# Optimization experiments

Hardware: AMD Instinct MI355X
Metric: run time of the kernel (lower is better)

Reference implementation:

```python
import jax, jax.numpy as jnp
import numpy as np

B, L, DIM = 2, 2048, 512
HEADS, R, W, EH, T = 8, 8, 4, 16, 2
HD = DIM // HEADS  # 64
ROPE_BASE = 10000.0


def _local_window_edges(L, w):
    pos = np.arange(L)
    offs = np.concatenate([np.arange(-w, 0), np.arange(1, w + 1)])
    tg = pos[:, None] + offs[None, :]
    valid = (tg >= 0) & (tg < L)
    ii, _ = np.nonzero(valid)          # row-major, matches torch nonzero order
    return ii.astype(np.int32), tg[valid].astype(np.int32)


def setup_inputs() -> dict:
    key = jax.random.key(0)
    ks = jax.random.split(key, 12)
    sd = 0.02
    edge_i, edge_j = _local_window_edges(L, W)
    inp = {
        "x": jax.random.normal(ks[0], (B, L, DIM), jnp.float32),
        "edge_i": jnp.asarray(edge_i),
        "edge_j": jnp.asarray(edge_j),
        "te_w": jax.random.normal(ks[1], (DIM, DIM), jnp.float32) * sd,
        "te_b": jnp.zeros((DIM,), jnp.float32),
        "a1_w": jax.random.normal(ks[2], (2 * DIM, EH), jnp.float32) * sd,
        "a1_b": jnp.zeros((EH,), jnp.float32),
        "a2_w": jax.random.normal(ks[3], (EH, 1), jnp.float32) * sd,
        "a2_b": jnp.zeros((1,), jnp.float32),
        "l1_w": jax.random.normal(ks[4], (2 * DIM, EH), jnp.float32) * sd,
        "l1_b": jnp.zeros((EH,), jnp.float32),
        "l2_w": jax.random.normal(ks[5], (EH, HEADS * R * HD), jnp.float32) * sd,
        "l2_b": jnp.zeros((HEADS * R * HD,), jnp.float32),
        "step_sizes": jnp.full((T, L), -2.2, jnp.float32),
        "out_w": jax.random.normal(ks[6], (DIM, DIM), jnp.float32) * sd,
        "out_b": jnp.zeros((DIM,), jnp.float32),
    }
    return inp


def _rope_cos_sin(rel_pos):
    # rel_pos: [E] int -> cos/sin [E, HD] (rotate-half convention)
    inv_freq = 1.0 / (ROPE_BASE ** (jnp.arange(0, HD, 2, dtype=jnp.float32) / HD))
    ang = rel_pos.astype(jnp.float32)[:, None] * inv_freq[None, :]  # [E, HD/2]
    ang = jnp.concatenate([ang, ang], axis=-1)                      # [E, HD]
    return jnp.cos(ang), jnp.sin(ang)


def _rotate_half(x):
    x1, x2 = x[..., : HD // 2], x[..., HD // 2:]
    return jnp.concatenate([-x2, x1], axis=-1)


def reference(x, edge_i, edge_j, te_w, te_b, a1_w, a1_b, a2_w, a2_b,
              l1_w, l1_b, l2_w, l2_b, step_sizes, out_w, out_b):
    E = edge_i.shape[0]
    # token encoder -> heads: u [B, H, L, HD]
    u = (x @ te_w + te_b).reshape(B, L, HEADS, HD).transpose(0, 2, 1, 3)

    # edge features from raw x: [B, E, 2*DIM]
    ef = jnp.concatenate([x[:, edge_i], x[:, edge_j]], axis=-1)
    # alpha: softplus MLP -> [B, E]
    h = jax.nn.gelu(ef @ a1_w + a1_b, approximate=False)
    alphas = jax.nn.softplus((h @ a2_w + a2_b)[..., 0])
    # Lambda: MLP -> [B, E, H, R, HD], L2-normalized on last dim
    h2 = jax.nn.gelu(ef @ l1_w + l1_b, approximate=False)
    Lam = (h2 @ l2_w + l2_b).reshape(B, E, HEADS, R, HD)
    Lam = Lam / jnp.maximum(jnp.linalg.norm(Lam, axis=-1, keepdims=True), 1e-12)

    cos, sin = _rope_cos_sin(edge_i - edge_j)  # [E, HD] each

    for t in range(T):
        eta = jax.nn.softplus(step_sizes[t])[None, None, :, None]  # [1,1,L,1]
        u_i = u[:, :, edge_i]                                      # [B,H,E,HD]
        u_j = u[:, :, edge_j]
        u_i = u_i * cos + _rotate_half(u_i) * sin
        diff = u_i - u_j
        ld = jnp.einsum('behrd,bhed->bher', Lam, diff)
        residual = alphas[:, None, :, None] * diff + jnp.einsum('bher,behrd->bhed', ld, Lam)
        upd = jnp.zeros_like(u).at[:, :, edge_i, :].add(residual)
        upd = upd.at[:, :, edge_j, :].add(-residual)
        u = u - eta * upd

    u = u.transpose(0, 2, 1, 3).reshape(B, L, DIM)
    return u @ out_w + out_b
```

## Files before the change

kernel.cpp:

```cpp
#include <hip/hip_runtime.h>
#include <hip/hip_bf16.h>

#define B_   2
#define L_   2048
#define DIM_ 512
#define NH_  8
#define HD_  64
#define R_   8
#define EH_  16
#define T_   2

__device__ __forceinline__ float gelu_f(float x){
  return 0.5f * x * (1.0f + erff(x * 0.70710678118654752f));
}
__device__ __forceinline__ float softplus_f(float x){
  return (x > 20.f) ? x : log1pf(expf(x));
}
__device__ __forceinline__ constexpr int off_of(int o){ return (o < 4) ? o - 4 : o - 3; }

__global__ __launch_bounds__(256) void k_misc(
    const float* __restrict__ l2w, const float* __restrict__ l2b,
    const float* __restrict__ step,
    float* __restrict__ W2, float* __restrict__ eta,
    float* __restrict__ ropeC, float* __restrict__ ropeS,
    int* __restrict__ esrc, int* __restrict__ edst)
{
  int idx = blockIdx.x * 256 + threadIdx.x;
  if (idx < NH_*144*64){
    int d = idx & 63;
    int n = (idx >> 6) % 144;
    int h = idx / (144*64);
    int k = n >> 3, r = n & 7;
    int col = h*512 + r*64 + d;
    float v = 0.f;
    if (k < 16) v = l2w[k*4096 + col];
    else if (k == 16) v = l2b[col];
    W2[idx] = v;
    return;
  }
  idx -= NH_*144*64;
  if (idx < T_*L_){ eta[idx] = softplus_f(step[idx]); return; }
  idx -= T_*L_;
  if (idx < 9*32){
    int d = idx & 31, rel = (idx >> 5) - 4;
    float invf = expf(-((float)d / 32.f) * 9.210340371976184f);
    float ang = (float)rel * invf;
    ropeC[idx] = cosf(ang); ropeS[idx] = sinf(ang);
    return;
  }
  idx -= 9*32;
  if (idx < 2*8*L_){
    if (idx < 8*L_) esrc[idx] = -1; else edst[idx - 8*L_] = -1;
    return;
  }
}

__global__ __launch_bounds__(256) void k_gram(
    const float* __restrict__ W2, float* __restrict__ Gram)
{
  int idx = blockIdx.x * 256 + threadIdx.x;
  if (idx >= 8*8*17*17) return;
  int bq = idx % 17;
  int a  = (idx / 17) % 17;
  int r  = (idx / 289) & 7;
  int h  = idx / (289*8);
  const float* wa = W2 + ((size_t)(h*144 + a*8 + r))*64;
  const float* wb = W2 + ((size_t)(h*144 + bq*8 + r))*64;
  float s = 0.f;
  #pragma unroll 8
  for (int d = 0; d < 64; d++) s = fmaf(wa[d], wb[d], s);
  Gram[idx] = s;
}

__global__ __launch_bounds__(256) void k_fill(
    const int* __restrict__ ei, const int* __restrict__ ej, int E,
    int* __restrict__ esrc, int* __restrict__ edst)
{
  int e = blockIdx.x * 256 + threadIdx.x;
  if (e >= E) return;
  int i = ei[e], j = ej[e];
  int o = j - i;
  int slot = (o < 0) ? (o + 4) : (o + 3);
  esrc[slot*L_ + i] = e;
  edst[slot*L_ + j] = e;
}

__global__ __launch_bounds__(256) void k_te(
    const float* __restrict__ x, const float* __restrict__ w,
    const float* __restrict__ bias, float* __restrict__ u)
{
  __shared__ float As[16][64];
  __shared__ float Bs[16][64];
  const int m0 = blockIdx.x * 64;
  const int n0 = blockIdx.y * 64;
  const int tid = threadIdx.x;
  const int ty = tid >> 4, tx = tid & 15;
  float acc[4][4] = {};
  for (int k0 = 0; k0 < 512; k0 += 16){
    {
      int m = tid >> 2, seg = tid & 3;
      float4 v = *(const float4*)(x + (size_t)(m0 + m)*512 + k0 + seg*4);
      As[seg*4+0][m] = v.x; As[seg*4+1][m] = v.y;
      As[seg*4+2][m] = v.z; As[seg*4+3][m] = v.w;
    }
    {
      int k = tid >> 4, c = (tid & 15)*4;
      float4 v = *(const float4*)(w + (size_t)(k0 + k)*512 + n0 + c);
      *(float4*)&Bs[k][c] = v;
    }
    __syncthreads();
    #pragma unroll
    for (int k = 0; k < 16; k++){
      float4 a = *(const float4*)(&As[k][ty*4]);
      float4 b = *(const float4*)(&Bs[k][tx*4]);
      float av[4] = {a.x, a.y, a.z, a.w};
      float bv[4] = {b.x, b.y, b.z, b.w};
      #pragma unroll
      for (int ii = 0; ii < 4; ii++)
        #pragma unroll
        for (int jj = 0; jj < 4; jj++)
          acc[ii][jj] = fmaf(av[ii], bv[jj], acc[ii][jj]);
    }
    __syncthreads();
  }
  const int bb = m0 >> 11;
  const int lb = (m0 & 2047) + ty*4;
  #pragma unroll
  for (int jj = 0; jj < 4; jj++){
    int n = n0 + tx*4 + jj;
    float bv = bias[n];
    float4 o;
    o.x = acc[0][jj] + bv; o.y = acc[1][jj] + bv;
    o.z = acc[2][jj] + bv; o.w = acc[3][jj] + bv;
    *(float4*)&u[((size_t)(bb*512 + n))*2048 + lb] = o;
  }
}

__global__ __launch_bounds__(256) void k_pq(
    const float* __restrict__ x, const float* __restrict__ a1w,
    const float* __restrict__ l1w, float* __restrict__ PQ)
{
  __shared__ float As[16][64];
  __shared__ float Bs[16][64];
  const int m0 = blockIdx.x * 64;
  const int tid = threadIdx.x;
  const int ty = tid >> 4, tx = tid & 15;
  const int c = (tid & 15) * 4;
  const int group = c >> 4;
  const float* src = (group & 2) ? l1w : a1w;
  const int krow_off = (group & 1) ? 512 : 0;
  const int cc = c & 15;
  float acc[4][4] = {};
  for (int k0 = 0; k0 < 512; k0 += 16){
    {
      int m = tid >> 2, seg = tid & 3;
      float4 v = *(const float4*)(x + (size_t)(m0 + m)*512 + k0 + seg*4);
      As[seg*4+0][m] = v.x; As[seg*4+1][m] = v.y;
      As[seg*4+2][m] = v.z; As[seg*4+3][m] = v.w;
    }
    {
      int k = tid >> 4;
      float4 v = *(const float4*)(src + (size_t)(krow_off + k0 + k)*16 + cc);
      *(float4*)&Bs[k][c] = v;
    }
    __syncthreads();
    #pragma unroll
    for (int k = 0; k < 16; k++){
      float4 a = *(const float4*)(&As[k][ty*4]);
      float4 b = *(const float4*)(&Bs[k][tx*4]);
      float av[4] = {a.x, a.y, a.z, a.w};
      float bv[4] = {b.x, b.y, b.z, b.w};
      #pragma unroll
      for (int ii = 0; ii < 4; ii++)
        #pragma unroll
        for (int jj = 0; jj < 4; jj++)
          acc[ii][jj] = fmaf(av[ii], bv[jj], acc[ii][jj]);
    }
    __syncthreads();
  }
  #pragma unroll
  for (int ii = 0; ii < 4; ii++){
    int m = m0 + ty*4 + ii;
    float4 o;
    o.x = acc[ii][0]; o.y = acc[ii][1]; o.z = acc[ii][2]; o.w = acc[ii][3];
    *(float4*)&PQ[(size_t)m*64 + tx*4] = o;
  }
}

__global__ __launch_bounds__(256) void k_feat2(
    const float* __restrict__ PQ, const int* __restrict__ ei, const int* __restrict__ ej,
    const float* __restrict__ a1b, const float* __restrict__ a2w,
    const float* __restrict__ a2b, const float* __restrict__ l1b,
    int E, float* __restrict__ alphas, float* __restrict__ h2e)
{
  int e = blockIdx.x * 256 + threadIdx.x;
  int b = blockIdx.y;
  if (e >= E) return;
  int i = ei[e], j = ej[e];
  const float* Pi = PQ + ((size_t)b*L_ + i)*64;
  const float* Pj = PQ + ((size_t)b*L_ + j)*64;
  float ha[16], hl[16];
  #pragma unroll
  for (int q = 0; q < 4; q++){
    float4 p1 = *(const float4*)(Pi + q*4);
    float4 q1 = *(const float4*)(Pj + 16 + q*4);
    float4 p2 = *(const float4*)(Pi + 32 + q*4);
    float4 q2 = *(const float4*)(Pj + 48 + q*4);
    ha[q*4+0] = p1.x + q1.x; ha[q*4+1] = p1.y + q1.y;
    ha[q*4+2] = p1.z + q1.z; ha[q*4+3] = p1.w + q1.w;
    hl[q*4+0] = p2.x + q2.x; hl[q*4+1] = p2.y + q2.y;
    hl[q*4+2] = p2.z + q2.z; hl[q*4+3] = p2.w + q2.w;
  }
  float av = a2b[0];
  #pragma unroll
  for (int n = 0; n < 16; n++){
    float g = gelu_f(ha[n] + a1b[n]);
    av += g * a2w[n];
  }
  alphas[(size_t)b*E + e] = softplus_f(av);
  float* he = h2e + ((size_t)b*E + e)*16;
  #pragma unroll
  for (int n = 0; n < 16; n++){
    float g = gelu_f(hl[n] + l1b[n]);
    he[n] = g;
  }
}

__global__ __launch_bounds__(256) void k_norm(
    const float* __restrict__ Gram, const float* __restrict__ h2e,
    int E, float* __restrict__ ivsq)
{
  __shared__ float Gl[8*289];
  __shared__ float Hl[256*17];
  const int tid = threadIdx.x;
  const int bh = blockIdx.y;
  const int b = bh >> 3, h = bh & 7;
  const int eb = blockIdx.x*256;
  for (int it = tid; it < 2312; it += 256) Gl[it] = Gram[(size_t)h*2312 + it];
  {
    int ge = eb + tid;
    const float* hp = h2e + ((size_t)b*E + (ge < E ? ge : 0))*16;
    #pragma unroll
    for (int q = 0; q < 4; q++){
      float4 v = *(const float4*)(hp + q*4);
      Hl[tid*17+q*4+0]=v.x; Hl[tid*17+q*4+1]=v.y;
      Hl[tid*17+q*4+2]=v.z; Hl[tid*17+q*4+3]=v.w;
    }
    Hl[tid*17+16] = 1.f;
  }
  __syncthreads();
  int ge = eb + tid;
  if (ge >= E) return;
  float m17[17];
  #pragma unroll
  for (int k = 0; k < 17; k++) m17[k] = Hl[tid*17+k];
  float* ig = ivsq + ((size_t)bh*E + ge)*8;
  #pragma unroll
  for (int r = 0; r < 8; r++){
    float ss = 0.f;
    for (int a = 0; a < 17; a++){
      float ma = Hl[tid*17 + a];
      const float* Gr = Gl + r*289 + a*17;
      float inner = 0.f;
      #pragma unroll
      for (int bq = 0; bq < 17; bq++)
        inner = fmaf(m17[bq], Gr[bq], inner);
      ss = fmaf(ma, inner, ss);
    }
    ig[r] = 1.f / fmaxf(ss, 1e-24f);
  }
}

__global__ __launch_bounds__(256) void k_S(
    const float* __restrict__ u, const float* __restrict__ W2,
    const float* __restrict__ h2e,
    const float* __restrict__ ropeC, const float* __restrict__ ropeS,
    const int* __restrict__ ei, const int* __restrict__ ej,
    int E, const float* __restrict__ ivsq, float* __restrict__ coefg)
{
  __shared__ float Wl[136*64];
  __shared__ float Hl[256*17];
  __shared__ float rCT[288], rST[288];
  const int tid = threadIdx.x;
  const int bh = blockIdx.y;
  const int b = bh >> 3, h = bh & 7;
  const int eb = blockIdx.x*256;

  {
    const float* Wg = W2 + (size_t)h*144*64;
    for (int fi = tid; fi < 136*16; fi += 256){
      int n = fi >> 4, kq = (fi & 15)*4;
      *(float4*)&Wl[n*64 + kq] = *(const float4*)(Wg + (size_t)n*64 + kq);
    }
  }
  for (int it = tid; it < 288; it += 256){
    int rix = it >> 5, p = it & 31;
    rCT[p*9 + rix] = ropeC[it];
    rST[p*9 + rix] = ropeS[it];
  }
  {
    int ge = eb + tid;
    const float* hp = h2e + ((size_t)b*E + (ge < E ? ge : 0))*16;
    #pragma unroll
    for (int q = 0; q < 4; q++){
      float4 v = *(const float4*)(hp + q*4);
      Hl[tid*17+q*4+0]=v.x; Hl[tid*17+q*4+1]=v.y;
      Hl[tid*17+q*4+2]=v.z; Hl[tid*17+q*4+3]=v.w;
    }
    Hl[tid*17+16] = 1.f;
  }
  __syncthreads();

  const int dq = tid & 3;
  const int qd = tid >> 2;
  const int e0 = eb + qd*4;
  const int el0 = qd*4;
  const int p0 = 8*dq;

  int iiv[4], jjv[4], rxv[4];
  #pragma unroll
  for (int s = 0; s < 4; s++){
    int ge = e0 + s;
    int gi = (ge < E) ? ge : (E-1);
    iiv[s] = ei[gi]; jjv[s] = ej[gi];
    rxv[s] = iiv[s] - jjv[s] + 4;
  }
  const float* ub = u + ((size_t)(b*512 + h*64))*2048;

  float dA[4][8], dB[4][8];
  #pragma unroll
  for (int s = 0; s < 4; s++){
    #pragma unroll
    for (int q = 0; q < 8; q++){
      int dp = p0 + q;
      float c  = rCT[dp*9 + rxv[s]];
      float sn = rST[dp*9 + rxv[s]];
      float ui0 = ub[(size_t)dp*2048 + iiv[s]];
      float ui1 = ub[(size_t)(dp+32)*2048 + iiv[s]];
      float uj0 = ub[(size_t)dp*2048 + jjv[s]];
      float uj1 = ub[(size_t)(dp+32)*2048 + jjv[s]];
      dA[s][q] = ui0*c - ui1*sn - uj0;
      dB[s][q] = ui1*c + ui0*sn - uj1;
    }
  }

  float P[4][8] = {};
  for (int k = 0; k < 17; k++){
    float mk0 = Hl[(el0+0)*17 + k];
    float mk1 = Hl[(el0+1)*17 + k];
    float mk2 = Hl[(el0+2)*17 + k];
    float mk3 = Hl[(el0+3)*17 + k];
    const float* wk = Wl + (k*8)*64 + p0;
    #pragma unroll
    for (int r = 0; r < 8; r++){
      const float* wr = wk + r*64;
      float4 a0 = *(const float4*)(wr);
      float4 a1 = *(const float4*)(wr + 4);
      float4 b0 = *(const float4*)(wr + 32);
      float4 b1 = *(const float4*)(wr + 36);
      #pragma unroll
      for (int s = 0; s < 4; s++){
        float pd;
        pd = dA[s][0]*a0.x;
        pd = fmaf(dA[s][1], a0.y, pd);
        pd = fmaf(dA[s][2], a0.z, pd);
        pd = fmaf(dA[s][3], a0.w, pd);
        pd = fmaf(dA[s][4], a1.x, pd);
        pd = fmaf(dA[s][5], a1.y, pd);
        pd = fmaf(dA[s][6], a1.z, pd);
        pd = fmaf(dA[s][7], a1.w, pd);
        pd = fmaf(dB[s][0], b0.x, pd);
        pd = fmaf(dB[s][1], b0.y, pd);
        pd = fmaf(dB[s][2], b0.z, pd);
        pd = fmaf(dB[s][3], b0.w, pd);
        pd = fmaf(dB[s][4], b1.x, pd);
        pd = fmaf(dB[s][5], b1.y, pd);
        pd = fmaf(dB[s][6], b1.z, pd);
        pd = fmaf(dB[s][7], b1.w, pd);
        float mk = (s==0)?mk0:(s==1)?mk1:(s==2)?mk2:mk3;
        P[s][r] = fmaf(mk, pd, P[s][r]);
      }
    }
  }

  #pragma unroll
  for (int s = 0; s < 4; s++)
    #pragma unroll
    for (int r = 0; r < 8; r++){
      float v = P[s][r];
      v += __shfl_xor(v, 1);
      v += __shfl_xor(v, 2);
      P[s][r] = v;
    }

  int ge = e0 + dq;
  if (ge < E){
    float S8[8];
    #pragma unroll
    for (int r = 0; r < 8; r++){
      float v0 = P[0][r], v1 = P[1][r], v2 = P[2][r], v3 = P[3][r];
      S8[r] = (dq==0) ? v0 : (dq==1) ? v1 : (dq==2) ? v2 : v3;
    }
    const float* ig = ivsq + ((size_t)bh*E + ge)*8;
    float* cg = coefg + ((size_t)bh*E + ge)*8;
    #pragma unroll
    for (int r = 0; r < 8; r++) cg[r] = ig[r]*S8[r];
  }
}

__global__ __launch_bounds__(256) void k_apply(
    const float* __restrict__ uin, float* __restrict__ uout,
    const float* __restrict__ W2,
    const float* __restrict__ h2e, const float* __restrict__ coefg,
    const float* __restrict__ alphas,
    const float* __restrict__ ropeC, const float* __restrict__ ropeS,
    const int* __restrict__ esrc, const int* __restrict__ edst,
    const int* __restrict__ ei, const int* __restrict__ ej,
    const float* __restrict__ eta, int E, int t)
{
  __shared__ float smem[10816];
  float* Al  = smem;
  float* UtF = smem;
  float* SaF = smem + 4896;
  int*   Es  = (int*)(smem + 9216);
  float* rCl = smem + 10240;
  float* rSl = smem + 10528;

  const int tid = threadIdx.x;
  const int l0 = blockIdx.x * 64;
  const int bh = blockIdx.y;
  const int b = bh >> 3, h = bh & 7;
  const float* ub = uin + ((size_t)(b*512 + h*64))*2048;
  float*       uo = uout + ((size_t)(b*512 + h*64))*2048;
  const float* Wg = W2 + (size_t)h*144*64;

  #pragma unroll
  for (int it = 0; it < 4; it++){
    int si = it*256 + tid;
    int o = si >> 6, ll = si & 63;
    Es[si] = (o < 8) ? esrc[o*L_ + l0 + ll] : edst[(o-8)*L_ + l0 + ll];
  }
  for (int it = tid; it < 288; it += 256){ rCl[it] = ropeC[it]; rSl[it] = ropeS[it]; }
  for (int it = tid; it < 9216; it += 256) Al[it] = 0.f;
  __syncthreads();

  {
    const int l = tid & 63;
    const int kc = tid >> 6;
    const int kbase = kc*4;
    float areg[5][8];
    #pragma unroll
    for (int k = 0; k < 5; k++)
      #pragma unroll
      for (int r = 0; r < 8; r++) areg[k][r] = 0.f;
    for (int o = 0; o < 16; o++){
      int e = Es[o*64 + l];
      if (e < 0) continue;
      float sign = (o < 8) ? 1.f : -1.f;
      const float* hp = h2e + ((size_t)b*E + e)*16;
      const float* cp = coefg + ((size_t)bh*E + e)*8;
      float4 m4 = *(const float4*)(hp + kbase);
      float4 c0 = *(const float4*)cp;
      float4 c1 = *(const float4*)(cp + 4);
      float cf[8] = {c0.x, c0.y, c0.z, c0.w, c1.x, c1.y, c1.z, c1.w};
      float smv[4] = {sign*m4.x, sign*m4.y, sign*m4.z, sign*m4.w};
      #pragma unroll
      for (int k = 0; k < 4; k++)
        #pragma unroll
        for (int r = 0; r < 8; r++)
          areg[k][r] = fmaf(smv[k], cf[r], areg[k][r]);
      if (kc == 3){
        #pragma unroll
        for (int r = 0; r < 8; r++) areg[4][r] += sign*cf[r];
      }
    }
    const int sw = (l >> 2) & 3;
    #pragma unroll
    for (int k = 0; k < 4; k++){
      #pragma unroll
      for (int r = 0; r < 8; r++){
        int n = (kbase + k)*8 + r;
        Al[l*144 + (((n >> 2) ^ sw) << 2) + (n & 3)] = areg[k][r];
      }
    }
    if (kc == 3){
      #pragma unroll
      for (int r = 0; r < 8; r++){
        int n = 128 + r;
        Al[l*144 + (((n >> 2) ^ sw) << 2) + (n & 3)] = areg[4][r];
      }
    }
  }
  __syncthreads();

  const int lg = tid & 15, dg = tid >> 4;
  float acc[4][4] = {};
  {
    const int swr = lg & 3;
    for (int nf4 = 0; nf4 < 34; nf4++){
      int sf4 = (nf4 ^ swr) << 2;
      float4 Av[4];
      #pragma unroll
      for (int tt = 0; tt < 4; tt++)
        Av[tt] = *(const float4*)&Al[(lg*4 + tt)*144 + sf4];
      int n = nf4*4;
      #pragma unroll
      for (int q = 0; q < 4; q++){
        float4 wb = *(const float4*)(Wg + (size_t)(n + q)*64 + dg*4);
        #pragma unroll
        for (int tt = 0; tt < 4; tt++){
          float a = (q==0)?Av[tt].x:(q==1)?Av[tt].y:(q==2)?Av[tt].z:Av[tt].w;
          acc[tt][0] = fmaf(a, wb.x, acc[tt][0]);
          acc[tt][1] = fmaf(a, wb.y, acc[tt][1]);
          acc[tt][2] = fmaf(a, wb.z, acc[tt][2]);
          acc[tt][3] = fmaf(a, wb.w, acc[tt][3]);
        }
      }
    }
  }
  __syncthreads();

  #pragma unroll
  for (int it = 0; it < 18; it++){
    int flat = it*256 + tid;
    int d = flat / 72;
    int c = flat - d*72;
    int col = l0 - 4 + c;
    col = (col < 0) ? 0 : ((col > 2047) ? 2047 : col);
    UtF[c*68 + d] = ub[(size_t)d*2048 + col];
  }
  #pragma unroll
  for (int it = 0; it < 4; it++){
    int si = it*256 + tid;
    int e = Es[si];
    SaF[si] = (e >= 0) ? alphas[(size_t)b*E + e] : 0.f;
  }
  __syncthreads();

  const int pbase = (dg*4) & 31;
  const float sgn = (dg < 8) ? -1.f : 1.f;
  const int pcol = (dg*4 + 32) & 63;
  float4 rcv[8], rsv[8];
  #pragma unroll
  for (int o = 0; o < 8; o++){
    const int rix = 4 - off_of(o);
    rcv[o] = *(const float4*)&rCl[rix*32 + pbase];
    rsv[o] = *(const float4*)&rSl[rix*32 + pbase];
  }
  #pragma unroll
  for (int tt = 0; tt < 4; tt++){
    const int ll = lg*4 + tt;
    const int myl = l0 + ll;
    const int lrel = ll + 4;
    const float et = eta[t*L_ + myl];
    float4 ul  = *(const float4*)&UtF[lrel*68 + dg*4];
    float4 ulp = *(const float4*)&UtF[lrel*68 + pcol];
    float upd[4] = {acc[tt][0], acc[tt][1], acc[tt][2], acc[tt][3]};
    float ulv[4] = {ul.x, ul.y, ul.z, ul.w};
    float ulpv[4] = {ulp.x, ulp.y, ulp.z, ulp.w};
    #pragma unroll
    for (int o = 0; o < 8; o++){
      int e = Es[o*64 + ll];
      if (e >= 0){
        float al = SaF[o*64 + ll];
        float4 uj = *(const float4*)&UtF[(lrel + off_of(o))*68 + dg*4];
        float ujv[4] = {uj.x, uj.y, uj.z, uj.w};
        float rc[4] = {rcv[o].x, rcv[o].y, rcv[o].z, rcv[o].w};
        float rs[4] = {rsv[o].x, rsv[o].y, rsv[o].z, rsv[o].w};
        #pragma unroll
        for (int q = 0; q < 4; q++){
          float rope = rc[q]*ulv[q] + sgn*rs[q]*ulpv[q];
          upd[q] = fmaf(al, rope - ujv[q], upd[q]);
        }
      }
    }
    #pragma unroll
    for (int o = 0; o < 8; o++){
      int e = Es[(8 + o)*64 + ll];
      if (e >= 0){
        float al = SaF[(8 + o)*64 + ll];
        int lr2 = lrel - off_of(o);
        float4 ui  = *(const float4*)&UtF[lr2*68 + dg*4];
        float4 uip = *(const float4*)&UtF[lr2*68 + pcol];
        float uiv[4] = {ui.x, ui.y, ui.z, ui.w};
        float uipv[4] = {uip.x, uip.y, uip.z, uip.w};
        float rc[4] = {rcv[o].x, rcv[o].y, rcv[o].z, rcv[o].w};
        float rs[4] = {rsv[o].x, rsv[o].y, rsv[o].z, rsv[o].w};
        #pragma unroll
        for (int q = 0; q < 4; q++){
          float rope = rc[q]*uiv[q] + sgn*rs[q]*uipv[q];
          upd[q] -= al * (rope - ulv[q]);
        }
      }
    }
    #pragma unroll
    for (int q = 0; q < 4; q++)
      uo[(size_t)(dg*4 + q)*2048 + myl] = ulv[q] - et*upd[q];
  }
}

__global__ __launch_bounds__(256) void k_out(
    const float* __restrict__ u, const float* __restrict__ w,
    const float* __restrict__ bias, float* __restrict__ outp)
{
  __shared__ float As[16][64];
  __shared__ float Bs[16][64];
  const int m0 = blockIdx.x * 64;
  const int n0 = blockIdx.y * 64;
  const int tid = threadIdx.x;
  const int ty = tid >> 4, tx = tid & 15;
  const int bb = m0 >> 11;
  const int l0 = m0 & 2047;
  float acc[4][4] = {};
  for (int k0 = 0; k0 < 512; k0 += 16){
    {
      int k = tid >> 4, ls = (tid & 15)*4;
      float4 v = *(const float4*)&u[((size_t)(bb*512 + k0 + k))*2048 + l0 + ls];
      *(float4*)&As[k][ls] = v;
    }
    {
      int k = tid >> 4, c = (tid & 15)*4;
      float4 v = *(const float4*)(w + (size_t)(k0 + k)*512 + n0 + c);
      *(float4*)&Bs[k][c] = v;
    }
    __syncthreads();
    #pragma unroll
    for (int k = 0; k < 16; k++){
      float4 a = *(const float4*)(&As[k][ty*4]);
      float4 b = *(const float4*)(&Bs[k][tx*4]);
      float av[4] = {a.x, a.y, a.z, a.w};
      float bv[4] = {b.x, b.y, b.z, b.w};
      #pragma unroll
      for (int ii = 0; ii < 4; ii++)
        #pragma unroll
        for (int jj = 0; jj < 4; jj++)
          acc[ii][jj] = fmaf(av[ii], bv[jj], acc[ii][jj]);
    }
    __syncthreads();
  }
  float bv[4];
  #pragma unroll
  for (int jj = 0; jj < 4; jj++) bv[jj] = bias[n0 + tx*4 + jj];
  #pragma unroll
  for (int ii = 0; ii < 4; ii++){
    int l = l0 + ty*4 + ii;
    float4 o;
    o.x = acc[ii][0] + bv[0];
    o.y = acc[ii][1] + bv[1];
    o.z = acc[ii][2] + bv[2];
    o.w = acc[ii][3] + bv[3];
    *(float4*)&outp[((size_t)(bb*2048 + l))*512 + n0 + tx*4] = o;
  }
}

extern "C" void kernel_launch(void* const* d_in, const int* in_sizes, int n_in,
                              void* d_out, int out_size, void* d_ws, size_t ws_size,
                              hipStream_t stream)
{
  const float* x    = (const float*)d_in[0];
  const int*   ei   = (const int*)d_in[1];
  const int*   ej   = (const int*)d_in[2];
  const float* tew  = (const float*)d_in[3];
  const float* teb  = (const float*)d_in[4];
  const float* a1w  = (const float*)d_in[5];
  const float* a1b  = (const float*)d_in[6];
  const float* a2w  = (const float*)d_in[7];
  const float* a2b  = (const float*)d_in[8];
  const float* l1w  = (const float*)d_in[9];
  const float* l1b  = (const float*)d_in[10];
  const float* l2w  = (const float*)d_in[11];
  const float* l2b  = (const float*)d_in[12];
  const float* step = (const float*)d_in[13];
  const float* ow   = (const float*)d_in[14];
  const float* ob   = (const float*)d_in[15];
  float* outp = (float*)d_out;
  const int E = in_sizes[1];

  char* p = (char*)d_ws;
  auto carve = [&](size_t nbytes)->char*{
    char* q = p; p += (nbytes + 255) & ~(size_t)255; return q;
  };
  float* u0     = (float*)carve((size_t)B_*512*2048*4);
  float* u1     = (float*)carve((size_t)B_*512*2048*4);
  float* PQ     = (float*)carve((size_t)B_*L_*64*4);
  float* h2e    = (float*)carve((size_t)B_*E*16*4);
  float* alphas = (float*)carve((size_t)B_*E*4);
  float* coefg  = (float*)carve((size_t)B_*NH_*E*8*4);
  float* ivsq   = (float*)carve((size_t)B_*NH_*E*8*4);
  float* W2     = (float*)carve((size_t)NH_*144*64*4);
  float* Gram   = (float*)carve((size_t)8*8*17*17*4);
  float* eta    = (float*)carve((size_t)T_*L_*4);
  float* ropeC  = (float*)carve((size_t)288*4);
  float* ropeS  = (float*)carve((size_t)288*4);
  int*   esrc   = (int*)carve((size_t)8*L_*4);
  int*   edst   = (int*)carve((size_t)8*L_*4);

  {
    int total = NH_*144*64 + T_*L_ + 9*32 + 2*8*L_;
    k_misc<<<dim3((total + 255)/256), dim3(256), 0, stream>>>(
        l2w, l2b, step, W2, eta, ropeC, ropeS, esrc, edst);
  }
  k_gram<<<dim3((8*8*17*17 + 255)/256), dim3(256), 0, stream>>>(W2, Gram);
  k_fill<<<dim3((E + 255)/256), dim3(256), 0, stream>>>(ei, ej, E, esrc, edst);
  k_te<<<dim3(64, 8), dim3(256), 0, stream>>>(x, tew, teb, u0);
  k_pq<<<dim3(64), dim3(256), 0, stream>>>(x, a1w, l1w, PQ);
  k_feat2<<<dim3((E + 255)/256, B_), dim3(256), 0, stream>>>(
      PQ, ei, ej, a1b, a2w, a2b, l1b, E, alphas, h2e);

  const int etiles = (E + 255)/256;
  k_norm<<<dim3(etiles, B_*NH_), dim3(256), 0, stream>>>(Gram, h2e, E, ivsq);

  float* ucur = u0;
  float* unxt = u1;
  for (int t = 0; t < T_; t++){
    k_S<<<dim3(etiles, B_*NH_), dim3(256), 0, stream>>>(
        ucur, W2, h2e, ropeC, ropeS, ei, ej, E, ivsq, coefg);
    k_apply<<<dim3(L_/64, B_*NH_), dim3(256), 0, stream>>>(
        ucur, unxt, W2, h2e, coefg, alphas, ropeC, ropeS,
        esrc, edst, ei, ej, eta, E, t);
    float* tmp = ucur; ucur = unxt; unxt = tmp;
  }

  k_out<<<dim3(64, 8), dim3(256), 0, stream>>>(ucur, ow, ob, outp);
}
```

Baseline: 365.1 us.

## Process eight edges per thread in k_S with transposed global edge features

Each k_S thread group now handles eight edges instead of four, so each block covers 512 edges and every shared-memory load of W2 feeds twice as many FMAs. The edge MLP hidden features are written by k_feat2 in an extra transposed buffer, so k_S reads them as coalesced float4s straight from global memory instead of staging them in shared memory. The constant bias term is peeled out of the k loop. The cost is a much larger register footprint (dA, dB and P double) and half as many blocks, which may reduce occupancy or cause spills.

```diff
diff --git a/kernel.cpp b/kernel.cpp
--- a/kernel.cpp
+++ b/kernel.cpp
@@ -191,7 +191,8 @@
     const float* __restrict__ PQ, const int* __restrict__ ei, const int* __restrict__ ej,
     const float* __restrict__ a1b, const float* __restrict__ a2w,
     const float* __restrict__ a2b, const float* __restrict__ l1b,
-    int E, float* __restrict__ alphas, float* __restrict__ h2e)
+    int E, float* __restrict__ alphas, float* __restrict__ h2e,
+    float* __restrict__ h2t)
 {
   int e = blockIdx.x * 256 + threadIdx.x;
   int b = blockIdx.y;
@@ -223,6 +224,7 @@
   for (int n = 0; n < 16; n++){
     float g = gelu_f(hl[n] + l1b[n]);
     he[n] = g;
+    h2t[((size_t)b*16 + n)*E + e] = g;
   }
 }
 
@@ -273,18 +275,17 @@
 
 __global__ __launch_bounds__(256) void k_S(
     const float* __restrict__ u, const float* __restrict__ W2,
-    const float* __restrict__ h2e,
+    const float* __restrict__ h2t,
     const float* __restrict__ ropeC, const float* __restrict__ ropeS,
     const int* __restrict__ ei, const int* __restrict__ ej,
     int E, const float* __restrict__ ivsq, float* __restrict__ coefg)
 {
   __shared__ float Wl[136*64];
-  __shared__ float Hl[256*17];
   __shared__ float rCT[288], rST[288];
   const int tid = threadIdx.x;
   const int bh = blockIdx.y;
   const int b = bh >> 3, h = bh & 7;
-  const int eb = blockIdx.x*256;
+  const int eb = blockIdx.x*512;
 
   {
     const float* Wg = W2 + (size_t)h*144*64;
@@ -298,58 +299,41 @@
     rCT[p*9 + rix] = ropeC[it];
     rST[p*9 + rix] = ropeS[it];
   }
-  {
-    int ge = eb + tid;
-    const float* hp = h2e + ((size_t)b*E + (ge < E ? ge : 0))*16;
-    #pragma unroll
-    for (int q = 0; q < 4; q++){
-      float4 v = *(const float4*)(hp + q*4);
-      Hl[tid*17+q*4+0]=v.x; Hl[tid*17+q*4+1]=v.y;
-      Hl[tid*17+q*4+2]=v.z; Hl[tid*17+q*4+3]=v.w;
-    }
-    Hl[tid*17+16] = 1.f;
-  }
   __syncthreads();
 
   const int dq = tid & 3;
   const int qd = tid >> 2;
-  const int e0 = eb + qd*4;
-  const int el0 = qd*4;
+  const int e0 = eb + qd*8;
   const int p0 = 8*dq;
-
-  int iiv[4], jjv[4], rxv[4];
-  #pragma unroll
-  for (int s = 0; s < 4; s++){
+  const float* ub = u + ((size_t)(b*512 + h*64))*2048;
+  const float* h2b = h2t + (size_t)b*16*E;
+
+  float dA[8][8], dB[8][8];
+  #pragma unroll
+  for (int s = 0; s < 8; s++){
     int ge = e0 + s;
     int gi = (ge < E) ? ge : (E-1);
-    iiv[s] = ei[gi]; jjv[s] = ej[gi];
-    rxv[s] = iiv[s] - jjv[s] + 4;
-  }
-  const float* ub = u + ((size_t)(b*512 + h*64))*2048;
-
-  float dA[4][8], dB[4][8];
-  #pragma unroll
-  for (int s = 0; s < 4; s++){
+    int ii = ei[gi], jj = ej[gi];
+    int rx = ii - jj + 4;
     #pragma unroll
     for (int q = 0; q < 8; q++){
       int dp = p0 + q;
-      float c  = rCT[dp*9 + rxv[s]];
-      float sn = rST[dp*9 + rxv[s]];
-      float ui0 = ub[(size_t)dp*2048 + iiv[s]];
-      float ui1 = ub[(size_t)(dp+32)*2048 + iiv[s]];
-      float uj0 = ub[(size_t)dp*2048 + jjv[s]];
-      float uj1 = ub[(size_t)(dp+32)*2048 + jjv[s]];
+      float c  = rCT[dp*9 + rx];
+      float sn = rST[dp*9 + rx];
+      float ui0 = ub[(size_t)dp*2048 + ii];
+      float ui1 = ub[(size_t)(dp+32)*2048 + ii];
+      float uj0 = ub[(size_t)dp*2048 + jj];
+      float uj1 = ub[(size_t)(dp+32)*2048 + jj];
       dA[s][q] = ui0*c - ui1*sn - uj0;
       dB[s][q] = ui1*c + ui0*sn - uj1;
     }
   }
 
-  float P[4][8] = {};
-  for (int k = 0; k < 17; k++){
-    float mk0 = Hl[(el0+0)*17 + k];
-    float mk1 = Hl[(el0+1)*17 + k];
-    float mk2 = Hl[(el0+2)*17 + k];
-    float mk3 = Hl[(el0+3)*17 + k];
+  float P[8][8] = {};
+  for (int k = 0; k < 16; k++){
+    float4 m0 = *(const float4*)(h2b + (size_t)k*E + e0);
+    float4 m1 = *(const float4*)(h2b + (size_t)k*E + e0 + 4);
+    float mk[8] = {m0.x, m0.y, m0.z, m0.w, m1.x, m1.y, m1.z, m1.w};
     const float* wk = Wl + (k*8)*64 + p0;
     #pragma unroll
     for (int r = 0; r < 8; r++){
@@ -359,7 +343,7 @@
       float4 b0 = *(const float4*)(wr + 32);
       float4 b1 = *(const float4*)(wr + 36);
       #pragma unroll
-      for (int s = 0; s < 4; s++){
+      for (int s = 0; s < 8; s++){
         float pd;
         pd = dA[s][0]*a0.x;
         pd = fmaf(dA[s][1], a0.y, pd);
@@ -377,14 +361,45 @@
         pd = fmaf(dB[s][5], b1.y, pd);
         pd = fmaf(dB[s][6], b1.z, pd);
         pd = fmaf(dB[s][7], b1.w, pd);
-        float mk = (s==0)?mk0:(s==1)?mk1:(s==2)?mk2:mk3;
-        P[s][r] = fmaf(mk, pd, P[s][r]);
-      }
-    }
-  }
-
-  #pragma unroll
-  for (int s = 0; s < 4; s++)
+        P[s][r] = fmaf(mk[s], pd, P[s][r]);
+      }
+    }
+  }
+  {
+    const float* wk = Wl + (16*8)*64 + p0;
+    #pragma unroll
+    for (int r = 0; r < 8; r++){
+      const float* wr = wk + r*64;
+      float4 a0 = *(const float4*)(wr);
+      float4 a1 = *(const float4*)(wr + 4);
+      float4 b0 = *(const float4*)(wr + 32);
+      float4 b1 = *(const float4*)(wr + 36);
+      #pragma unroll
+      for (int s = 0; s < 8; s++){
+        float pd;
+        pd = dA[s][0]*a0.x;
+        pd = fmaf(dA[s][1], a0.y, pd);
+        pd = fmaf(dA[s][2], a0.z, pd);
+        pd = fmaf(dA[s][3], a0.w, pd);
+        pd = fmaf(dA[s][4], a1.x, pd);
+        pd = fmaf(dA[s][5], a1.y, pd);
+        pd = fmaf(dA[s][6], a1.z, pd);
+        pd = fmaf(dA[s][7], a1.w, pd);
+        pd = fmaf(dB[s][0], b0.x, pd);
+        pd = fmaf(dB[s][1], b0.y, pd);
+        pd = fmaf(dB[s][2], b0.z, pd);
+        pd = fmaf(dB[s][3], b0.w, pd);
+        pd = fmaf(dB[s][4], b1.x, pd);
+        pd = fmaf(dB[s][5], b1.y, pd);
+        pd = fmaf(dB[s][6], b1.z, pd);
+        pd = fmaf(dB[s][7], b1.w, pd);
+        P[s][r] += pd;
+      }
+    }
+  }
+
+  #pragma unroll
+  for (int s = 0; s < 8; s++)
     #pragma unroll
     for (int r = 0; r < 8; r++){
       float v = P[s][r];
@@ -393,18 +408,19 @@
       P[s][r] = v;
     }
 
-  int ge = e0 + dq;
-  if (ge < E){
-    float S8[8];
-    #pragma unroll
-    for (int r = 0; r < 8; r++){
-      float v0 = P[0][r], v1 = P[1][r], v2 = P[2][r], v3 = P[3][r];
-      S8[r] = (dq==0) ? v0 : (dq==1) ? v1 : (dq==2) ? v2 : v3;
-    }
-    const float* ig = ivsq + ((size_t)bh*E + ge)*8;
-    float* cg = coefg + ((size_t)bh*E + ge)*8;
-    #pragma unroll
-    for (int r = 0; r < 8; r++) cg[r] = ig[r]*S8[r];
+  #pragma unroll
+  for (int z = 0; z < 2; z++){
+    int ge = e0 + dq*2 + z;
+    if (ge < E){
+      const float* ig = ivsq + ((size_t)bh*E + ge)*8;
+      float* cg = coefg + ((size_t)bh*E + ge)*8;
+      #pragma unroll
+      for (int r = 0; r < 8; r++){
+        float v = (dq==0) ? P[0+z][r] : (dq==1) ? P[2+z][r]
+                : (dq==2) ? P[4+z][r] : P[6+z][r];
+        cg[r] = ig[r]*v;
+      }
+    }
   }
 }
 
@@ -684,6 +700,7 @@
   float* u1     = (float*)carve((size_t)B_*512*2048*4);
   float* PQ     = (float*)carve((size_t)B_*L_*64*4);
   float* h2e    = (float*)carve((size_t)B_*E*16*4);
+  float* h2t    = (float*)carve((size_t)(B_*16*E + 64)*4);
   float* alphas = (float*)carve((size_t)B_*E*4);
   float* coefg  = (float*)carve((size_t)B_*NH_*E*8*4);
   float* ivsq   = (float*)carve((size_t)B_*NH_*E*8*4);
@@ -705,16 +722,16 @@
   k_te<<<dim3(64, 8), dim3(256), 0, stream>>>(x, tew, teb, u0);
   k_pq<<<dim3(64), dim3(256), 0, stream>>>(x, a1w, l1w, PQ);
   k_feat2<<<dim3((E + 255)/256, B_), dim3(256), 0, stream>>>(
-      PQ, ei, ej, a1b, a2w, a2b, l1b, E, alphas, h2e);
-
-  const int etiles = (E + 255)/256;
-  k_norm<<<dim3(etiles, B_*NH_), dim3(256), 0, stream>>>(Gram, h2e, E, ivsq);
-
+      PQ, ei, ej, a1b, a2w, a2b, l1b, E, alphas, h2e, h2t);
+
+  k_norm<<<dim3((E + 255)/256, B_*NH_), dim3(256), 0, stream>>>(Gram, h2e, E, ivsq);
+
+  const int etiles = (E + 511)/512;
   float* ucur = u0;
   float* unxt = u1;
   for (int t = 0; t < T_; t++){
     k_S<<<dim3(etiles, B_*NH_), dim3(256), 0, stream>>>(
-        ucur, W2, h2e, ropeC, ropeS, ei, ej, E, ivsq, coefg);
+        ucur, W2, h2t, ropeC, ropeS, ei, ej, E, ivsq, coefg);
     k_apply<<<dim3(L_/64, B_*NH_), dim3(256), 0, stream>>>(
         ucur, unxt, W2, h2e, coefg, alphas, ropeC, ropeS,
         esrc, edst, ei, ej, eta, E, t);
```

Result: slower. 999.0 us (+173.6%).
